# Optimization experiments

Hardware: AMD Instinct MI355X
Metric: run time of the kernel (lower is better)

The kernel has to match this reference:

```python
import jax, jax.numpy as jnp
import numpy as np

T1 = 0.2
T2 = 1.2
LABEL_SMOOTHING = 0.05
NUM_ITERS = 20  # fixed-point iterations for lambda_t_a (t2 > 1 branch)


def log_t(x, t):
    # tempered log (t != 1)
    return (x ** (1.0 - t) - 1.0) / (1.0 - t)


def exp_t(x, t):
    # tempered exp (t != 1): relu((1-t)x + 1) ** (1/(1-t))
    return jnp.maximum((1.0 - t) * x + 1.0, 0.0) ** (1.0 / (1.0 - t))


def lambda_t_a(a, t):
    # t > 1 fixed-point branch of the original torch code, with a fixed
    # iteration count instead of a host-synced convergence check.
    mu = jnp.max(a, axis=-1, keepdims=True)            # [N, 1]
    norm_a_initial = a - mu                            # [N, C], <= 0

    def body(norm_a, _):
        z_a = jnp.sum(exp_t(norm_a, t), axis=-1, keepdims=True)  # [N, 1]
        return z_a ** (1.0 - t) * norm_a_initial, None

    norm_a, _ = jax.lax.scan(body, norm_a_initial, None, length=NUM_ITERS)
    z_a = jnp.sum(exp_t(norm_a, t), axis=-1, keepdims=True)
    return -log_t(1.0 / z_a, t) + mu                   # [N, 1]


def setup_inputs() -> dict:
    key = jax.random.key(0)
    k1, k2 = jax.random.split(key)
    N, C = 16384, 1000
    inputs = jax.random.normal(k1, (N, C), dtype=jnp.float32)
    labels = jax.random.randint(k2, (N,), 0, C)
    targets = jax.nn.one_hot(labels, C, dtype=jnp.float32)
    return {"inputs": inputs, "targets": targets}


def reference(inputs, targets):
    num_classes = targets.shape[-1]
    # label smoothing (label_smoothing > 0 branch)
    targets = (1.0 - num_classes / (num_classes - 1) * LABEL_SMOOTHING) * targets \
              + LABEL_SMOOTHING / (num_classes - 1)
    norm_constants = lambda_t_a(inputs, T2)                      # [N, 1]
    probabilities = exp_t(inputs - norm_constants, T2)           # [N, C]
    loss1 = targets * (log_t(targets + 1e-8, T1) - log_t(probabilities, T1))
    loss2 = (targets ** (2.0 - T1) - probabilities ** (2.0 - T1)) / (2.0 - T1)
    out = jnp.sum(loss1 - loss2, axis=-1)                        # [N]
    return jnp.mean(out)
```

## Files before the change

kernel.cpp:

```cpp
#include <hip/hip_runtime.h>
#include <math.h>
#include <stdint.h>

#define C_DIM 1000
#define BIG   1.0e30f

typedef float fx4 __attribute__((ext_vector_type(4)));

typedef __attribute__((address_space(1))) void g_void;
typedef __attribute__((address_space(3))) void l_void;

__device__ __forceinline__ float fexp2(float x) { return __builtin_amdgcn_exp2f(x); }
__device__ __forceinline__ float flog2(float x) { return __builtin_amdgcn_logf(x); }
__device__ __forceinline__ float frcp(float x)  { return __builtin_amdgcn_rcpf(x); }

__device__ __forceinline__ void gll16(const float* g, float* l) {
    __builtin_amdgcn_global_load_lds((g_void*)g, (l_void*)l, 16, 0, 0);
}

template <int CTRL, int RM>
__device__ __forceinline__ float dpp_add_term(float x) {
    int y = __builtin_amdgcn_update_dpp(0, __float_as_int(x), CTRL, RM, 0xf, true);
    return __int_as_float(y);
}
template <int CTRL, int RM>
__device__ __forceinline__ float dpp_max_term(float x) {
    int y = __builtin_amdgcn_update_dpp(__float_as_int(x), __float_as_int(x), CTRL, RM, 0xf, false);
    return __int_as_float(y);
}

#define DPP_SUM_CHAIN(x)                      \
    x += dpp_add_term<0x111, 0xf>(x);         \
    x += dpp_add_term<0x112, 0xf>(x);         \
    x += dpp_add_term<0x114, 0xf>(x);         \
    x += dpp_add_term<0x118, 0xf>(x);         \
    x += dpp_add_term<0x142, 0xa>(x);         \
    x += dpp_add_term<0x143, 0xc>(x);

__device__ __forceinline__ float bcast63(float x) {
    return __int_as_float(__builtin_amdgcn_readlane(__float_as_int(x), 63));
}

__device__ __forceinline__ float wave_sum(float x) {
    DPP_SUM_CHAIN(x)
    return bcast63(x);
}

__device__ __forceinline__ float wave_max(float x) {
    x = fmaxf(x, dpp_max_term<0x111, 0xf>(x));
    x = fmaxf(x, dpp_max_term<0x112, 0xf>(x));
    x = fmaxf(x, dpp_max_term<0x114, 0xf>(x));
    x = fmaxf(x, dpp_max_term<0x118, 0xf>(x));
    x = fmaxf(x, dpp_max_term<0x142, 0xa>(x));
    x = fmaxf(x, dpp_max_term<0x143, 0xc>(x));
    return bcast63(x);
}

__device__ __forceinline__ float tr16(const fx4 x0, const fx4 x1,
                                      const fx4 x2, const fx4 x3,
                                      float bb[16])
{
    bb[0]=-0.2f*x0.x;  bb[1]=-0.2f*x0.y;  bb[2]=-0.2f*x0.z;  bb[3]=-0.2f*x0.w;
    bb[4]=-0.2f*x1.x;  bb[5]=-0.2f*x1.y;  bb[6]=-0.2f*x1.z;  bb[7]=-0.2f*x1.w;
    bb[8]=-0.2f*x2.x;  bb[9]=-0.2f*x2.y;  bb[10]=-0.2f*x2.z; bb[11]=-0.2f*x2.w;
    bb[12]=-0.2f*x3.x; bb[13]=-0.2f*x3.y; bb[14]=-0.2f*x3.z; bb[15]=-0.2f*x3.w;
    float m0 = fmaxf(fmaxf(x0.x, x0.y), fmaxf(x0.z, x0.w));
    float m1 = fmaxf(fmaxf(x1.x, x1.y), fmaxf(x1.z, x1.w));
    float m2 = fmaxf(fmaxf(x2.x, x2.y), fmaxf(x2.z, x2.w));
    float m3 = fmaxf(fmaxf(x3.x, x3.y), fmaxf(x3.z, x3.w));
    return fmaxf(fmaxf(m0, m1), fmaxf(m2, m3));
}

__device__ __forceinline__ float dot16(const fx4 t0, const fx4 t1,
                                       const fx4 t2, const fx4 t3,
                                       const float bb[16])
{
    float s = 0.0f;
    s = fmaf(t0.x, bb[0],  s); s = fmaf(t0.y, bb[1],  s);
    s = fmaf(t0.z, bb[2],  s); s = fmaf(t0.w, bb[3],  s);
    s = fmaf(t1.x, bb[4],  s); s = fmaf(t1.y, bb[5],  s);
    s = fmaf(t1.z, bb[6],  s); s = fmaf(t1.w, bb[7],  s);
    s = fmaf(t2.x, bb[8],  s); s = fmaf(t2.y, bb[9],  s);
    s = fmaf(t2.z, bb[10], s); s = fmaf(t2.w, bb[11], s);
    s = fmaf(t3.x, bb[12], s); s = fmaf(t3.y, bb[13], s);
    s = fmaf(t3.z, bb[14], s); s = fmaf(t3.w, bb[15], s);
    return s;
}

__device__ __forceinline__ void row_core(const float bb[16], float mxl, float ahbl,
                                         float* __restrict__ row_out, int row, int lane,
                                         bool st, float C0, float E_off, float dE)
{
    const float mu  = wave_max(mxl);
    const float ahb = wave_sum(ahbl);
    const float g   = 0.2f * mu;
    const float hb  = ahb + g;

    const float c1 = 1.0f + g;
    float s = 0.0f;
    #pragma unroll
    for (int k = 0; k < 16; ++k) {
        float u = bb[k] + c1;
        float u2 = u * u;
        s += frcp(u2 * u2 * u);
    }
    s = wave_sum(s);
    const float lam = fexp2(-0.2f * flog2(s));

    const float c2 = fmaf(lam, g, 1.0f);
    s = 0.0f;
    #pragma unroll
    for (int k = 0; k < 16; ++k) {
        float u = fmaf(lam, bb[k], c2);
        float u2 = u * u;
        s += frcp(u2 * u2 * u);
    }
    s = wave_sum(s);
    const float w = fexp2(0.2f * flog2(s));

    const float c3 = w + g;
    float S4 = 0.0f, S5 = 0.0f, S6 = 0.0f, S9 = 0.0f, S10 = 0.0f, S11 = 0.0f;
    #pragma unroll
    for (int k = 0; k < 16; ++k) {
        float r  = frcp(bb[k] + c3);
        float r2 = r * r;
        float r4 = r2 * r2;
        float r5 = r4 * r;
        float r9 = r4 * r5;
        S4  += r4;
        S5  += r5;
        S6  += r5 * r;
        S9  += r9;
        S10 += r5 * r5;
        S11 += r9 * r2;
    }
    DPP_SUM_CHAIN(S4)
    DPP_SUM_CHAIN(S5)
    DPP_SUM_CHAIN(S6)
    DPP_SUM_CHAIN(S9)
    DPP_SUM_CHAIN(S10)
    DPP_SUM_CHAIN(S11)
    S4 = bcast63(S4);  S5 = bcast63(S5);  S6 = bcast63(S6);
    S9 = bcast63(S9);  S10 = bcast63(S10); S11 = bcast63(S11);

    const float d   = (S5 - 1.0f) * 0.2f * frcp(S6);
    const float w1  = w + d;
    const float d2  = d * d;
    const float S4c = S4 + fmaf(10.0f * d2, S6,  -4.0f * d * S5);
    const float S9c = S9 + fmaf(45.0f * d2, S11, -9.0f * d * S10);
    const float rh  = frcp(w1 + hb);
    const float rh2 = rh * rh;
    const float rh4 = rh2 * rh2;

    const float loss = fmaf(-E_off, S4c,
                       fmaf(-dE, rh4,
                       fmaf(1.0f / 1.8f, S9c, C0)));
    if (st && lane == 0) row_out[row] = loss;
}

__global__ __launch_bounds__(256, 8) void btll(
    const float* __restrict__ inputs, const float* __restrict__ targets,
    float* __restrict__ row_out, int n_rows,
    float C0, float E_off, float dE)
{
    const int lane = threadIdx.x & 63;
    const int wave = threadIdx.x >> 6;
    const int wid  = blockIdx.x * 4 + wave;
    const int r0i  = wid * 2;
    if (r0i >= n_rows) return;
    int r1i = r0i + 1;
    const bool st1 = r1i < n_rows;
    if (!st1) r1i = r0i;

    __shared__ __align__(16) float ldsT[4][1024];
    float* lt = &ldsT[wave][0];

    const float* in0 = inputs  + (size_t)r0i * C_DIM;
    const float* tg0 = targets + (size_t)r0i * C_DIM;
    const float* in1 = inputs  + (size_t)r1i * C_DIM;
    const float* tg1 = targets + (size_t)r1i * C_DIM;

    const bool m3 = lane < 58;
    const int  o3 = m3 ? (768 + 4 * lane) : 0;
    const fx4  xpad = (fx4){-BIG, -BIG, -BIG, -BIG};
    const fx4  zero = (fx4){0.f, 0.f, 0.f, 0.f};

    fx4 x0 = *(const fx4*)(in0 + 4 * lane);
    fx4 x1 = *(const fx4*)(in0 + 256 + 4 * lane);
    fx4 x2 = *(const fx4*)(in0 + 512 + 4 * lane);
    fx4 x3 = *(const fx4*)(in0 + o3);
    gll16(tg0 + 4 * lane,       lt);
    gll16(tg0 + 256 + 4 * lane, lt + 256);
    gll16(tg0 + 512 + 4 * lane, lt + 512);
    gll16(tg0 + o3,             lt + 768);

    x3 = m3 ? x3 : xpad;
    float bbA[16], bbB[16];
    float mx = tr16(x0, x1, x2, x3, bbA);

    asm volatile("s_waitcnt vmcnt(0)" ::: "memory");
    fx4 tv0 = *(const fx4*)(lt + 4 * lane);
    fx4 tv1 = *(const fx4*)(lt + 256 + 4 * lane);
    fx4 tv2 = *(const fx4*)(lt + 512 + 4 * lane);
    fx4 tv3 = *(const fx4*)(lt + 768 + 4 * lane);
    tv3 = m3 ? tv3 : zero;
    float ah = dot16(tv0, tv1, tv2, tv3, bbA);

    gll16(tg1 + 4 * lane,       lt);
    gll16(tg1 + 256 + 4 * lane, lt + 256);
    gll16(tg1 + 512 + 4 * lane, lt + 512);
    gll16(tg1 + o3,             lt + 768);
    fx4 p0, p1, p2, p3;
    {
        const float* a0 = in1 + 4 * lane;
        const float* a1 = in1 + 256 + 4 * lane;
        const float* a2 = in1 + 512 + 4 * lane;
        const float* a3 = in1 + o3;
        asm volatile("global_load_dwordx4 %0, %1, off" : "=v"(p0) : "v"(a0));
        asm volatile("global_load_dwordx4 %0, %1, off" : "=v"(p1) : "v"(a1));
        asm volatile("global_load_dwordx4 %0, %1, off" : "=v"(p2) : "v"(a2));
        asm volatile("global_load_dwordx4 %0, %1, off" : "=v"(p3) : "v"(a3));
    }
    asm volatile("" ::: "memory");

    row_core(bbA, mx, ah, row_out, r0i, lane, true, C0, E_off, dE);

    asm volatile("s_waitcnt vmcnt(1)"
                 : "+v"(p0), "+v"(p1), "+v"(p2), "+v"(p3) :: "memory");
    p3 = m3 ? p3 : xpad;
    mx = tr16(p0, p1, p2, p3, bbB);
    tv0 = *(const fx4*)(lt + 4 * lane);
    tv1 = *(const fx4*)(lt + 256 + 4 * lane);
    tv2 = *(const fx4*)(lt + 512 + 4 * lane);
    tv3 = *(const fx4*)(lt + 768 + 4 * lane);
    tv3 = m3 ? tv3 : zero;
    ah = dot16(tv0, tv1, tv2, tv3, bbB);

    row_core(bbB, mx, ah, row_out, r1i, lane, st1, C0, E_off, dE);
}

__global__ __launch_bounds__(1024) void reduce_mean(
    const float* __restrict__ row_out, float* __restrict__ out, int n)
{
    __shared__ double sm[16];
    const int lane = threadIdx.x & 63;
    const int wv   = threadIdx.x >> 6;
    const int n4   = n >> 2;
    const float4* r4 = (const float4*)row_out;
    double s = 0.0;
    for (int i = threadIdx.x; i < n4; i += 1024) {
        float4 v = r4[i];
        s += (double)v.x + (double)v.y + (double)v.z + (double)v.w;
    }
    if (threadIdx.x == 0)
        for (int i = n4 << 2; i < n; ++i) s += (double)row_out[i];
    #pragma unroll
    for (int off = 32; off > 0; off >>= 1) s += __shfl_xor(s, off, 64);
    if (lane == 0) sm[wv] = s;
    __syncthreads();
    if (wv == 0) {
        double t = (lane < 16) ? sm[lane] : 0.0;
        #pragma unroll
        for (int off = 32; off > 0; off >>= 1) t += __shfl_xor(t, off, 64);
        if (lane == 0) out[0] = (float)(t / (double)n);
    }
}

extern "C" void kernel_launch(void* const* d_in, const int* in_sizes, int n_in,
                              void* d_out, int out_size, void* d_ws, size_t ws_size,
                              hipStream_t stream) {
    const float* inputs  = (const float*)d_in[0];
    const float* targets = (const float*)d_in[1];
    float* out = (float*)d_out;

    const int N = in_sizes[0] / C_DIM;
    float* row_out = (float*)d_ws;

    const double ls    = 0.05;
    const double c1g_d = 1.0 - (1000.0 / 999.0) * ls;
    const double c2_d  = ls / 999.0;
    const float  tp_on_f  = (float)c1g_d + (float)c2_d;
    const float  tp_off_f = (float)c2_d;
    const double tp_on  = (double)tp_on_f;
    const double tp_off = (double)tp_off_f;
    const double A_on  = (pow(tp_on  + 1e-8, 0.8) - 1.0) / 0.8;
    const double A_off = (pow(tp_off + 1e-8, 0.8) - 1.0) / 0.8;
    const double B_on  = pow(tp_on,  1.8);
    const double B_off = pow(tp_off, 1.8);
    const double E_on_d  = 1.25 * tp_on;
    const double E_off_d = 1.25 * tp_off;
    const double F_on_d  = tp_on  * A_on  + E_on_d  - B_on  / 1.8;
    const double F_off_d = tp_off * A_off + E_off_d - B_off / 1.8;
    const double C0_d    = (C_DIM - 1) * F_off_d + F_on_d;
    const double dE_d    = E_on_d - E_off_d;

    dim3 grid((N + 7) / 8);
    btll<<<grid, 256, 0, stream>>>(inputs, targets, row_out, N,
                                   (float)C0_d, (float)E_off_d, (float)dE_d);
    reduce_mean<<<1, 1024, 0, stream>>>(row_out, out, N);
}
```

Measured before the change: 146.5 us.

## Process four rows per wave with double-buffered prefetch of inputs and targets

```diff
diff --git a/kernel.cpp b/kernel.cpp
--- a/kernel.cpp
+++ b/kernel.cpp
@@ -16,6 +16,19 @@
 
 __device__ __forceinline__ void gll16(const float* g, float* l) {
     __builtin_amdgcn_global_load_lds((g_void*)g, (l_void*)l, 16, 0, 0);
+}
+
+__device__ __forceinline__ fx4 gload(const float* p) {
+    fx4 r;
+    asm volatile("global_load_dwordx4 %0, %1, off" : "=v"(r) : "v"(p));
+    return r;
+}
+
+__device__ __forceinline__ void wait8(fx4& a, fx4& b, fx4& c, fx4& d) {
+    asm volatile("s_waitcnt vmcnt(8)" : "+v"(a), "+v"(b), "+v"(c), "+v"(d) :: "memory");
+}
+__device__ __forceinline__ void wait0(fx4& a, fx4& b, fx4& c, fx4& d) {
+    asm volatile("s_waitcnt vmcnt(0)" : "+v"(a), "+v"(b), "+v"(c), "+v"(d) :: "memory");
 }
 
 template <int CTRL, int RM>
@@ -85,6 +98,34 @@
     s = fmaf(t3.x, bb[12], s); s = fmaf(t3.y, bb[13], s);
     s = fmaf(t3.z, bb[14], s); s = fmaf(t3.w, bb[15], s);
     return s;
+}
+
+__device__ __forceinline__ void prep(fx4 X0, fx4 X1, fx4 X2, fx4 X3,
+                                     const float* lt, int ol, bool m3,
+                                     float bb[16], float& mx, float& ah)
+{
+    X3 = m3 ? X3 : (fx4){-BIG, -BIG, -BIG, -BIG};
+    mx = tr16(X0, X1, X2, X3, bb);
+    fx4 v0 = *(const fx4*)(lt + ol);
+    fx4 v1 = *(const fx4*)(lt + 256 + ol);
+    fx4 v2 = *(const fx4*)(lt + 512 + ol);
+    fx4 v3 = *(const fx4*)(lt + 768 + ol);
+    v3 = m3 ? v3 : (fx4){0.f, 0.f, 0.f, 0.f};
+    ah = dot16(v0, v1, v2, v3, bb);
+}
+
+__device__ __forceinline__ void issue_row(const float* in_r, const float* tg_r,
+                                          int ol, int o3, float* lt,
+                                          fx4& X0, fx4& X1, fx4& X2, fx4& X3)
+{
+    X0 = gload(in_r + ol);
+    X1 = gload(in_r + 256 + ol);
+    X2 = gload(in_r + 512 + ol);
+    X3 = gload(in_r + o3);
+    gll16(tg_r + ol,       lt);
+    gll16(tg_r + 256 + ol, lt + 256);
+    gll16(tg_r + 512 + ol, lt + 512);
+    gll16(tg_r + o3,       lt + 768);
 }
 
 __device__ __forceinline__ void row_core(const float bb[16], float mxl, float ahbl,
@@ -158,7 +199,7 @@
     if (st && lane == 0) row_out[row] = loss;
 }
 
-__global__ __launch_bounds__(256, 8) void btll(
+__global__ __launch_bounds__(256, 4) void btll(
     const float* __restrict__ inputs, const float* __restrict__ targets,
     float* __restrict__ row_out, int n_rows,
     float C0, float E_off, float dE)
@@ -166,77 +207,57 @@
     const int lane = threadIdx.x & 63;
     const int wave = threadIdx.x >> 6;
     const int wid  = blockIdx.x * 4 + wave;
-    const int r0i  = wid * 2;
-    if (r0i >= n_rows) return;
-    int r1i = r0i + 1;
-    const bool st1 = r1i < n_rows;
-    if (!st1) r1i = r0i;
-
-    __shared__ __align__(16) float ldsT[4][1024];
-    float* lt = &ldsT[wave][0];
-
-    const float* in0 = inputs  + (size_t)r0i * C_DIM;
-    const float* tg0 = targets + (size_t)r0i * C_DIM;
-    const float* in1 = inputs  + (size_t)r1i * C_DIM;
-    const float* tg1 = targets + (size_t)r1i * C_DIM;
+    const int rb   = wid * 4;
+    if (rb >= n_rows) return;
+
+    const int r0 = rb;
+    const int r1 = min(rb + 1, n_rows - 1);
+    const int r2 = min(rb + 2, n_rows - 1);
+    const int r3 = min(rb + 3, n_rows - 1);
+    const bool st1 = (rb + 1) < n_rows;
+    const bool st2 = (rb + 2) < n_rows;
+    const bool st3 = (rb + 3) < n_rows;
+
+    __shared__ __align__(16) float ldsT[4][2][1024];
+    float* lt0 = &ldsT[wave][0][0];
+    float* lt1 = &ldsT[wave][1][0];
+
+    const float* i0p = inputs  + (size_t)r0 * C_DIM;
+    const float* t0p = targets + (size_t)r0 * C_DIM;
+    const float* i1p = inputs  + (size_t)r1 * C_DIM;
+    const float* t1p = targets + (size_t)r1 * C_DIM;
+    const float* i2p = inputs  + (size_t)r2 * C_DIM;
+    const float* t2p = targets + (size_t)r2 * C_DIM;
+    const float* i3p = inputs  + (size_t)r3 * C_DIM;
+    const float* t3p = targets + (size_t)r3 * C_DIM;
 
     const bool m3 = lane < 58;
-    const int  o3 = m3 ? (768 + 4 * lane) : 0;
-    const fx4  xpad = (fx4){-BIG, -BIG, -BIG, -BIG};
-    const fx4  zero = (fx4){0.f, 0.f, 0.f, 0.f};
-
-    fx4 x0 = *(const fx4*)(in0 + 4 * lane);
-    fx4 x1 = *(const fx4*)(in0 + 256 + 4 * lane);
-    fx4 x2 = *(const fx4*)(in0 + 512 + 4 * lane);
-    fx4 x3 = *(const fx4*)(in0 + o3);
-    gll16(tg0 + 4 * lane,       lt);
-    gll16(tg0 + 256 + 4 * lane, lt + 256);
-    gll16(tg0 + 512 + 4 * lane, lt + 512);
-    gll16(tg0 + o3,             lt + 768);
-
-    x3 = m3 ? x3 : xpad;
-    float bbA[16], bbB[16];
-    float mx = tr16(x0, x1, x2, x3, bbA);
-
-    asm volatile("s_waitcnt vmcnt(0)" ::: "memory");
-    fx4 tv0 = *(const fx4*)(lt + 4 * lane);
-    fx4 tv1 = *(const fx4*)(lt + 256 + 4 * lane);
-    fx4 tv2 = *(const fx4*)(lt + 512 + 4 * lane);
-    fx4 tv3 = *(const fx4*)(lt + 768 + 4 * lane);
-    tv3 = m3 ? tv3 : zero;
-    float ah = dot16(tv0, tv1, tv2, tv3, bbA);
-
-    gll16(tg1 + 4 * lane,       lt);
-    gll16(tg1 + 256 + 4 * lane, lt + 256);
-    gll16(tg1 + 512 + 4 * lane, lt + 512);
-    gll16(tg1 + o3,             lt + 768);
-    fx4 p0, p1, p2, p3;
-    {
-        const float* a0 = in1 + 4 * lane;
-        const float* a1 = in1 + 256 + 4 * lane;
-        const float* a2 = in1 + 512 + 4 * lane;
-        const float* a3 = in1 + o3;
-        asm volatile("global_load_dwordx4 %0, %1, off" : "=v"(p0) : "v"(a0));
-        asm volatile("global_load_dwordx4 %0, %1, off" : "=v"(p1) : "v"(a1));
-        asm volatile("global_load_dwordx4 %0, %1, off" : "=v"(p2) : "v"(a2));
-        asm volatile("global_load_dwordx4 %0, %1, off" : "=v"(p3) : "v"(a3));
-    }
-    asm volatile("" ::: "memory");
-
-    row_core(bbA, mx, ah, row_out, r0i, lane, true, C0, E_off, dE);
-
-    asm volatile("s_waitcnt vmcnt(1)"
-                 : "+v"(p0), "+v"(p1), "+v"(p2), "+v"(p3) :: "memory");
-    p3 = m3 ? p3 : xpad;
-    mx = tr16(p0, p1, p2, p3, bbB);
-    tv0 = *(const fx4*)(lt + 4 * lane);
-    tv1 = *(const fx4*)(lt + 256 + 4 * lane);
-    tv2 = *(const fx4*)(lt + 512 + 4 * lane);
-    tv3 = *(const fx4*)(lt + 768 + 4 * lane);
-    tv3 = m3 ? tv3 : zero;
-    ah = dot16(tv0, tv1, tv2, tv3, bbB);
-
-    row_core(bbB, mx, ah, row_out, r1i, lane, st1, C0, E_off, dE);
+    const int  ol = 4 * lane;
+    const int  o3 = m3 ? (768 + ol) : 0;
+
+    fx4 A0, A1, A2, A3, B0, B1, B2, B3;
+    float bb[16], mx, ah;
+
+    issue_row(i0p, t0p, ol, o3, lt0, A0, A1, A2, A3);
+    issue_row(i1p, t1p, ol, o3, lt1, B0, B1, B2, B3);
+    wait8(A0, A1, A2, A3);
+
+    prep(A0, A1, A2, A3, lt0, ol, m3, bb, mx, ah);
+    issue_row(i2p, t2p, ol, o3, lt0, A0, A1, A2, A3);
+    row_core(bb, mx, ah, row_out, r0, lane, true, C0, E_off, dE);
+    wait8(B0, B1, B2, B3);
+
+    prep(B0, B1, B2, B3, lt1, ol, m3, bb, mx, ah);
+    issue_row(i3p, t3p, ol, o3, lt1, B0, B1, B2, B3);
+    row_core(bb, mx, ah, row_out, r1, lane, st1, C0, E_off, dE);
+    wait8(A0, A1, A2, A3);
+
+    prep(A0, A1, A2, A3, lt0, ol, m3, bb, mx, ah);
+    row_core(bb, mx, ah, row_out, r2, lane, st2, C0, E_off, dE);
+    wait0(B0, B1, B2, B3);
+
+    prep(B0, B1, B2, B3, lt1, ol, m3, bb, mx, ah);
+    row_core(bb, mx, ah, row_out, r3, lane, st3, C0, E_off, dE);
 }
 
 __global__ __launch_bounds__(1024) void reduce_mean(
@@ -294,7 +315,7 @@
     const double C0_d    = (C_DIM - 1) * F_off_d + F_on_d;
     const double dE_d    = E_on_d - E_off_d;
 
-    dim3 grid((N + 7) / 8);
+    dim3 grid((N + 15) / 16);
     btll<<<grid, 256, 0, stream>>>(inputs, targets, row_out, N,
                                    (float)C0_d, (float)E_off_d, (float)dE_d);
     reduce_mean<<<1, 1024, 0, stream>>>(row_out, out, N);
```

After: 147.3 us. No clear change (+0.6%).
